# Kernel optimization log

Measured on AMD Instinct MI355X. Metric: run time of the kernel, lower is better.

## Reference

```python
import jax, jax.numpy as jnp
import numpy as np
import math

DIM = 1024
N_HEADS = 16
N_KV_HEADS = 8
HEAD_DIM = 64
HIDDEN = 4096
WINDOW = 512
NORM_EPS = 1e-5
QK_EPS = 1e-6


def get_alibi_slopes(n_heads):
    def _power_of_2(n):
        start = 2 ** (-2 ** (-(math.log2(n) - 3)))
        return [start * start ** i for i in range(n)]
    if math.log2(n_heads).is_integer():
        return _power_of_2(n_heads)
    closest = 2 ** math.floor(math.log2(n_heads))
    slopes = _power_of_2(closest)
    extra = _power_of_2(2 * closest)
    slopes.extend(extra[0::2][:n_heads - closest])
    return slopes


def layer_norm(x, w, eps):
    m = x.mean(-1, keepdims=True)
    v = ((x - m) ** 2).mean(-1, keepdims=True)
    return (x - m) * jax.lax.rsqrt(v + eps) * w


def setup_inputs() -> dict:
    key = jax.random.key(0)
    ks = jax.random.split(key, 16)
    s = 0.02
    return {
        "x": jax.random.normal(ks[0], (2, 2048, DIM), dtype=jnp.float32),
        "wq": jax.random.normal(ks[1], (N_HEADS * HEAD_DIM, DIM), dtype=jnp.float32) * s,
        "wk": jax.random.normal(ks[2], (N_KV_HEADS * HEAD_DIM, DIM), dtype=jnp.float32) * s,
        "wv": jax.random.normal(ks[3], (N_KV_HEADS * HEAD_DIM, DIM), dtype=jnp.float32) * s,
        "wo": jax.random.normal(ks[4], (DIM, N_HEADS * HEAD_DIM), dtype=jnp.float32) * s,
        "q_norm_w": jnp.ones((N_HEADS * HEAD_DIM,), dtype=jnp.float32),
        "k_norm_w": jnp.ones((N_KV_HEADS * HEAD_DIM,), dtype=jnp.float32),
        "attn_norm_w": jnp.ones((DIM,), dtype=jnp.float32),
        "ffn_norm_w": jnp.ones((DIM,), dtype=jnp.float32),
        "w1": jax.random.normal(ks[5], (HIDDEN, DIM), dtype=jnp.float32) * s,
        "w2": jax.random.normal(ks[6], (DIM, HIDDEN), dtype=jnp.float32) * s,
        "w3": jax.random.normal(ks[7], (HIDDEN, DIM), dtype=jnp.float32) * s,
        "attn_scale": jnp.full((DIM,), 1e-5, dtype=jnp.float32),
        "ffn_scale": jnp.full((DIM,), 1e-5, dtype=jnp.float32),
    }


def reference(x, wq, wk, wv, wo, q_norm_w, k_norm_w, attn_norm_w, ffn_norm_w,
              w1, w2, w3, attn_scale, ffn_scale):
    bsz, seqlen, _ = x.shape
    n_rep = N_HEADS // N_KV_HEADS

    h = layer_norm(x, attn_norm_w, NORM_EPS)
    q = layer_norm(h @ wq.T, q_norm_w, QK_EPS).reshape(bsz, seqlen, N_HEADS, HEAD_DIM).transpose(0, 2, 1, 3)
    k = layer_norm(h @ wk.T, k_norm_w, QK_EPS).reshape(bsz, seqlen, N_KV_HEADS, HEAD_DIM).transpose(0, 2, 1, 3)
    v = (h @ wv.T).reshape(bsz, seqlen, N_KV_HEADS, HEAD_DIM).transpose(0, 2, 1, 3)
    k = jnp.repeat(k, n_rep, axis=1)  # [b, H, s, hd]
    v = jnp.repeat(v, n_rep, axis=1)

    pos = jnp.arange(seqlen)
    dist = pos[None, :] - pos[:, None]  # dist[i, j] = j - i (as in the torch code)
    base = jnp.where((dist >= 0) & (dist <= WINDOW), 0.0, -jnp.inf)  # [s, s]
    slopes = jnp.asarray(get_alibi_slopes(N_HEADS), dtype=jnp.float32)
    alibi = -jnp.abs(slopes[:, None, None] * dist.astype(jnp.float32))  # [H, s, s]
    full_mask = base[None, :, :] + alibi  # [H, s, s]

    scores = jnp.einsum('bhqd,bhkd->bhqk', q, k) / math.sqrt(HEAD_DIM) + full_mask[None]
    attn = jax.nn.softmax(scores, axis=-1)
    out = jnp.einsum('bhqk,bhkd->bhqd', attn, v)
    out = out.transpose(0, 2, 1, 3).reshape(bsz, seqlen, N_HEADS * HEAD_DIM)
    x = x + (out @ wo.T) * attn_scale

    h2 = layer_norm(x, ffn_norm_w, NORM_EPS)
    ffn = (jax.nn.silu(h2 @ w1.T) * (h2 @ w3.T)) @ w2.T
    return x + ffn * ffn_scale
```

## Files before the change

kernel.cpp:

```cpp
#include <hip/hip_runtime.h>


typedef __bf16 bf16;
typedef __attribute__((ext_vector_type(8))) __bf16 bf16x8;
typedef __attribute__((ext_vector_type(4))) float f32x4;
typedef __attribute__((ext_vector_type(4))) short s16x4;

#define MFMA16(a, b, c) __builtin_amdgcn_mfma_f32_16x16x32_bf16(a, b, c, 0, 0, 0)

__device__ __forceinline__ void gload_lds16(const bf16* g, bf16* l) {
    __builtin_amdgcn_global_load_lds(
        (const __attribute__((address_space(1))) unsigned int*)g,
        (__attribute__((address_space(3))) unsigned int*)l, 16, 0, 0);
}

__global__ void sniff_kernel(const unsigned short* __restrict__ x, int* __restrict__ flag) {
    __shared__ int s;
    if (threadIdx.x == 0) s = 0;
    __syncthreads();
    int bad = 0;
#pragma unroll
    for (int i = 0; i < 16; ++i) {
        const unsigned short u = x[threadIdx.x * 16 + i];
        const int e = (u >> 7) & 0xFF;
        if (e >= 135) bad = 1;
    }
    if (bad) atomicOr(&s, 1);
    __syncthreads();
    if (threadIdx.x == 0) flag[0] = s;
}

__global__ void convert_all_kernel(const void* __restrict__ wq, const void* __restrict__ wk,
                                   const void* __restrict__ wv, const void* __restrict__ wo,
                                   const void* __restrict__ w1, const void* __restrict__ w3,
                                   const void* __restrict__ w2, bf16* __restrict__ dst,
                                   const int* __restrict__ flag) {
    const long e = ((long)blockIdx.x * 256 + threadIdx.x) * 4;
    const void* src; long off;
    if      (e < 1048576)  { src = wq; off = 0; }
    else if (e < 1572864)  { src = wk; off = 1048576; }
    else if (e < 2097152)  { src = wv; off = 1572864; }
    else if (e < 3145728)  { src = wo; off = 2097152; }
    else if (e < 7340032)  { src = w1; off = 3145728; }
    else if (e < 11534336) { src = w3; off = 7340032; }
    else                   { src = w2; off = 11534336; }
    if (flag[0] != 0) {
        const f32x4 v = *(const f32x4*)((const float*)src + (e - off));
        bf16 tmp[4];
#pragma unroll
        for (int j = 0; j < 4; ++j) tmp[j] = (bf16)v[j];
        *(s16x4*)(dst + e) = *(s16x4*)tmp;
    } else {
        *(s16x4*)(dst + e) = *(const s16x4*)((const short*)src + (e - off));
    }
}

__device__ __forceinline__ void ln_row(const void* in, const void* w, bf16* out,
                                       int row, int W, float eps, bool f32,
                                       int in_flv, int w_flv) {
    const int t = threadIdx.x;
    const int nch = W >> 3;
    const bool act = t < nch;
    float v[8];
    float s = 0.f, s2 = 0.f;
    if (act) {
        if (in_flv && f32) {
            const float* rp = (const float*)in + (size_t)row * W + t * 8;
            const f32x4 a = *(const f32x4*)rp, b = *(const f32x4*)(rp + 4);
#pragma unroll
            for (int j = 0; j < 4; ++j) { v[j] = a[j]; v[4 + j] = b[j]; }
        } else {
            const bf16x8 xv = *(const bf16x8*)((const bf16*)in + (size_t)row * W + t * 8);
#pragma unroll
            for (int j = 0; j < 8; ++j) v[j] = (float)xv[j];
        }
#pragma unroll
        for (int j = 0; j < 8; ++j) { s += v[j]; s2 += v[j] * v[j]; }
    }
#pragma unroll
    for (int off = 32; off; off >>= 1) { s += __shfl_xor(s, off); s2 += __shfl_xor(s2, off); }
    __shared__ float red[4];
    if ((t & 63) == 0) { red[(t >> 6) * 2] = s; red[(t >> 6) * 2 + 1] = s2; }
    __syncthreads();
    const float fs = red[0] + red[2], fs2 = red[1] + red[3];
    const float inw = 1.f / (float)W;
    const float mean = fs * inw;
    const float var = fs2 * inw - mean * mean;
    const float rstd = rsqrtf(var + eps);
    if (act) {
        float wv8[8];
        if (w_flv && f32) {
            const float* wp = (const float*)w + t * 8;
            const f32x4 a = *(const f32x4*)wp, b = *(const f32x4*)(wp + 4);
#pragma unroll
            for (int j = 0; j < 4; ++j) { wv8[j] = a[j]; wv8[4 + j] = b[j]; }
        } else {
            const bf16x8 ww = *(const bf16x8*)((const bf16*)w + t * 8);
#pragma unroll
            for (int j = 0; j < 8; ++j) wv8[j] = (float)ww[j];
        }
        bf16x8 ov;
#pragma unroll
        for (int j = 0; j < 8; ++j) ov[j] = (bf16)((v[j] - mean) * rstd * wv8[j]);
        *(bf16x8*)(out + (size_t)row * W + t * 8) = ov;
    }
}

__global__ void ln_kernel(const void* __restrict__ in, const void* __restrict__ w,
                          bf16* __restrict__ out, int W, float eps,
                          const int* __restrict__ flag, int in_flv, int w_flv) {
    ln_row(in, w, out, blockIdx.x, W, eps, flag[0] != 0, in_flv, w_flv);
}

__global__ void ln_qk_kernel(bf16* __restrict__ q, const void* __restrict__ qw,
                             bf16* __restrict__ kbuf, const void* __restrict__ kw,
                             const int* __restrict__ flag) {
    const bool f32 = flag[0] != 0;
    if (blockIdx.x < 4096)
        ln_row(q, qw, q, blockIdx.x, 1024, 1e-6f, f32, 0, 1);
    else
        ln_row(kbuf, kw, kbuf, blockIdx.x - 4096, 512, 1e-6f, f32, 0, 1);
}

__global__ void reduce_k(const bf16* __restrict__ p, const bf16* __restrict__ x1,
                         const void* __restrict__ scale, void* __restrict__ out,
                         const int* __restrict__ flag) {
    const bool f32 = flag[0] != 0;
    const size_t i8 = ((size_t)blockIdx.x * 256 + threadIdx.x) * 8;
    const int col = (int)(i8 & 1023);
    const bf16x8 a = *(const bf16x8*)(p + i8);
    const bf16x8 b = *(const bf16x8*)(p + 4194304 + i8);
    const bf16x8 r = *(const bf16x8*)(x1 + i8);
    float sc8[8];
    if (f32) {
        const f32x4 s0 = *(const f32x4*)((const float*)scale + col);
        const f32x4 s1 = *(const f32x4*)((const float*)scale + col + 4);
#pragma unroll
        for (int j = 0; j < 4; ++j) { sc8[j] = s0[j]; sc8[4 + j] = s1[j]; }
    } else {
        const bf16x8 sb = *(const bf16x8*)((const bf16*)scale + col);
#pragma unroll
        for (int j = 0; j < 8; ++j) sc8[j] = (float)sb[j];
    }
    float o[8];
#pragma unroll
    for (int j = 0; j < 8; ++j)
        o[j] = (float)r[j] + ((float)a[j] + (float)b[j]) * sc8[j];
    if (f32) {
        f32x4 o0, o1;
#pragma unroll
        for (int j = 0; j < 4; ++j) { o0[j] = o[j]; o1[j] = o[4 + j]; }
        *(f32x4*)((float*)out + i8) = o0;
        *(f32x4*)((float*)out + i8 + 4) = o1;
    } else {
        bf16x8 ov;
#pragma unroll
        for (int j = 0; j < 8; ++j) ov[j] = (bf16)o[j];
        *(bf16x8*)((bf16*)out + i8) = ov;
    }
}

template <int EPI, int NBUF, int SWZ, int SPLITK>
__global__ __launch_bounds__(512, 4)
void gemm2(const bf16* __restrict__ A, const bf16* __restrict__ B,
           void* __restrict__ Cout, const void* __restrict__ res,
           const void* __restrict__ scale, int M, int N, int K,
           const int* __restrict__ flag, int res_flv, int out_flv) {
    __shared__ bf16 LDS[NBUF * 8192];
    const bool f32 = flag[0] != 0;
    const int t = threadIdx.x;
    const int wv = t >> 6, ln = t & 63;
    const int qr = ln & 15, g = ln >> 4;
    const int wr = wv >> 2, wc = wv & 3;
    int bx = blockIdx.x, by = blockIdx.y;
    if (SWZ) {
        const int bid = by * gridDim.x + bx;
        const int g8 = bid & 7, m = bid >> 3;
        bx = m % gridDim.x;
        by = g8 + 8 * (m / gridDim.x);
    }
    const int row0 = by * 128, col0 = bx * 128;

    const int Koff = SPLITK ? (int)blockIdx.z * (K >> 1) : 0;
    const int Keff = SPLITK ? (K >> 1) : K;
    if (SPLITK) Cout = (void*)((bf16*)Cout + (size_t)blockIdx.z * ((size_t)M * N));

    f32x4 acc[4][2] = {};

    const int cx = ((t & 3) ^ ((t >> 2) & 3)) * 8;
    const bf16* aSrc = A + (size_t)(row0 + (t >> 2)) * K + Koff + cx;
    const bf16* bSrc = B + (size_t)(col0 + (t >> 2)) * K + Koff + cx;
    const int gx8 = (g ^ (qr & 3)) * 8;
    const int NIT = Keff >> 5;

#define STAGE(bi, k0)                                              \
    do {                                                           \
        bf16* lb = LDS + (bi) * 8192 + wv * 512;                   \
        gload_lds16(aSrc + (k0), lb);                              \
        gload_lds16(bSrc + (k0), lb + 4096);                       \
    } while (0)

#pragma unroll
    for (int pb = 0; pb < NBUF - 1; ++pb) STAGE(pb, pb * 32);
    if constexpr (NBUF == 3) asm volatile("s_waitcnt vmcnt(2)" ::: "memory");
    else                     asm volatile("s_waitcnt vmcnt(6)" ::: "memory");
    __builtin_amdgcn_s_barrier();
    __builtin_amdgcn_sched_barrier(0);

    int cur = 0, sb = NBUF - 1;
    for (int it = 0; it < NIT; ++it) {
        const bool more = (it + NBUF - 1) < NIT;
        if (more) STAGE(sb, (it + NBUF - 1) * 32);
        const bf16* bufA = LDS + cur * 8192;
        const bf16* bufB = bufA + 4096;
        bf16x8 af[4], bfr[2];
#pragma unroll
        for (int i = 0; i < 4; ++i)
            af[i] = *(const bf16x8*)&bufA[(wr * 64 + i * 16 + qr) * 32 + gx8];
#pragma unroll
        for (int j = 0; j < 2; ++j)
            bfr[j] = *(const bf16x8*)&bufB[(wc * 32 + j * 16 + qr) * 32 + gx8];
#pragma unroll
        for (int i = 0; i < 4; ++i)
#pragma unroll
            for (int j = 0; j < 2; ++j)
                acc[i][j] = MFMA16(af[i], bfr[j], acc[i][j]);
        if (more) {
            if constexpr (NBUF == 3) asm volatile("s_waitcnt vmcnt(2)" ::: "memory");
            else                     asm volatile("s_waitcnt vmcnt(6)" ::: "memory");
        } else {
            asm volatile("s_waitcnt vmcnt(0)" ::: "memory");
        }
        __builtin_amdgcn_s_barrier();
        __builtin_amdgcn_sched_barrier(0);
        cur = cur + 1 == NBUF ? 0 : cur + 1;
        sb  = sb + 1 == NBUF ? 0 : sb + 1;
    }
#undef STAGE

#pragma unroll
    for (int i = 0; i < 4; ++i) {
#pragma unroll
        for (int j = 0; j < 2; ++j) {
            const int rr0 = row0 + wr * 64 + i * 16 + g * 4;
            const int cc  = col0 + wc * 32 + j * 16 + qr;
            if (EPI == 4) {
                if (cc < 1024) {
#pragma unroll
                    for (int r = 0; r < 4; ++r)
                        ((bf16*)Cout)[(size_t)(rr0 + r) * 1024 + cc] = (bf16)acc[i][j][r];
                } else if (cc < 1536) {
#pragma unroll
                    for (int r = 0; r < 4; ++r)
                        ((bf16*)res)[(size_t)(rr0 + r) * 512 + (cc - 1024)] = (bf16)acc[i][j][r];
                } else {
                    const int kv = cc - 1536, kvh = kv >> 6, d = kv & 63;
                    const int bb = rr0 >> 11, s0 = rr0 & 2047;
                    bf16 tmp[4];
#pragma unroll
                    for (int r = 0; r < 4; ++r) tmp[r] = (bf16)acc[i][j][r];
                    *(s16x4*)((bf16*)scale + (((size_t)bb * 8 + kvh) * 64 + d) * 2048 + s0) = *(s16x4*)tmp;
                }
            } else {
                float scv = 0.f;
                if (EPI == 1)
                    scv = f32 ? ((const float*)scale)[cc] : (float)((const bf16*)scale)[cc];
#pragma unroll
                for (int r = 0; r < 4; ++r) {
                    const size_t idx = (size_t)(rr0 + r) * N + cc;
                    float vv = acc[i][j][r];
                    if (EPI == 1) {
                        const float rv = (res_flv && f32) ? ((const float*)res)[idx]
                                                          : (float)((const bf16*)res)[idx];
                        vv = rv + vv * scv;
                    }
                    if (EPI == 3) {
                        const float uv = (float)((const bf16*)res)[idx];
                        vv = uv / (1.f + __expf(-uv)) * vv;
                    }
                    if (out_flv && f32) ((float*)Cout)[idx] = vv;
                    else                ((bf16*)Cout)[idx] = (bf16)vv;
                }
            }
        }
    }
}

__global__ __launch_bounds__(512, 4)
void gemm_w13(const bf16* __restrict__ A, const bf16* __restrict__ B1,
              const bf16* __restrict__ B3, bf16* __restrict__ C,
              int M, int N, int K) {
    __shared__ bf16 LDS[3 * 12288];
    const int t = threadIdx.x;
    const int wv = t >> 6, ln = t & 63;
    const int qr = ln & 15, g = ln >> 4;
    const int wr = wv >> 2, wc = wv & 3;
    int bx, by;
    {
        const int bid = blockIdx.y * gridDim.x + blockIdx.x;
        const int xcd = bid & 7, m = bid >> 3;
        bx = xcd * 4 + (m & 3);
        by = m >> 2;
    }
    const int row0 = by * 128, col0 = bx * 128;

    f32x4 acc1[4][2] = {}, acc3[4][2] = {};

    const int cx = ((t & 3) ^ ((t >> 2) & 3)) * 8;
    const bf16* aSrc  = A  + (size_t)(row0 + (t >> 2)) * K + cx;
    const bf16* b1Src = B1 + (size_t)(col0 + (t >> 2)) * K + cx;
    const bf16* b3Src = B3 + (size_t)(col0 + (t >> 2)) * K + cx;
    const int gx8 = (g ^ (qr & 3)) * 8;
    const int NIT = K >> 5;

#define STAGEW(bi, k0)                                             \
    do {                                                           \
        bf16* lb = LDS + (bi) * 12288 + wv * 512;                  \
        gload_lds16(aSrc + (k0), lb);                              \
        gload_lds16(b1Src + (k0), lb + 4096);                      \
        gload_lds16(b3Src + (k0), lb + 8192);                      \
    } while (0)

    STAGEW(0, 0);
    STAGEW(1, 32);
    asm volatile("s_waitcnt vmcnt(3)" ::: "memory");
    __builtin_amdgcn_s_barrier();
    __builtin_amdgcn_sched_barrier(0);

    int cur = 0, sb = 2;
    for (int it = 0; it < NIT; ++it) {
        const bool more = (it + 2) < NIT;
        if (more) STAGEW(sb, (it + 2) * 32);
        const bf16* bufA  = LDS + cur * 12288;
        const bf16* bufB1 = bufA + 4096;
        const bf16* bufB3 = bufA + 8192;
        bf16x8 af[4], b1f[2], b3f[2];
#pragma unroll
        for (int i = 0; i < 4; ++i)
            af[i] = *(const bf16x8*)&bufA[(wr * 64 + i * 16 + qr) * 32 + gx8];
#pragma unroll
        for (int j = 0; j < 2; ++j) {
            b1f[j] = *(const bf16x8*)&bufB1[(wc * 32 + j * 16 + qr) * 32 + gx8];
            b3f[j] = *(const bf16x8*)&bufB3[(wc * 32 + j * 16 + qr) * 32 + gx8];
        }
#pragma unroll
        for (int i = 0; i < 4; ++i)
#pragma unroll
            for (int j = 0; j < 2; ++j) {
                acc1[i][j] = MFMA16(b1f[j], af[i], acc1[i][j]);
                acc3[i][j] = MFMA16(b3f[j], af[i], acc3[i][j]);
            }
        if (more) asm volatile("s_waitcnt vmcnt(3)" ::: "memory");
        else      asm volatile("s_waitcnt vmcnt(0)" ::: "memory");
        __builtin_amdgcn_s_barrier();
        __builtin_amdgcn_sched_barrier(0);
        cur = cur == 2 ? 0 : cur + 1;
        sb  = sb  == 2 ? 0 : sb  + 1;
    }
#undef STAGEW

#pragma unroll
    for (int i = 0; i < 4; ++i) {
        const int row = row0 + wr * 64 + i * 16 + qr;
#pragma unroll
        for (int j = 0; j < 2; ++j) {
            const int col = col0 + wc * 32 + j * 16 + g * 4;
            const size_t idx = (size_t)row * N + col;
            bf16 tmp[4];
#pragma unroll
            for (int r = 0; r < 4; ++r) {
                const float u1 = acc1[i][j][r];
                const float u3 = acc3[i][j][r];
                tmp[r] = (bf16)(u1 / (1.f + __expf(-u1)) * u3);
            }
            *(s16x4*)(C + idx) = *(s16x4*)tmp;
        }
    }
}

__global__ __launch_bounds__(512)
void attn_kernel(const bf16* __restrict__ qn, const bf16* __restrict__ kn,
                 const bf16* __restrict__ vt, bf16* __restrict__ aout) {
    __shared__ bf16 SH[3 * 4096];
    const int t = threadIdx.x, wv = t >> 6, ln = t & 63;
    const int qr = ln & 15, g = ln >> 4;
    const int kvh = blockIdx.y, b = blockIdx.z;
    const int hh = wv & 1, h = kvh * 2 + hh;
    const int qsub = wv >> 1;
    const int q0blk = blockIdx.x * 64;
    const int qa = q0blk + qsub * 16 + qr;
    const float slope = exp2f(-0.5f * (float)(h + 1));

    const bf16* qrow = qn + ((size_t)(b * 2048 + qa)) * 1024 + h * 64;
    const bf16x8 qb0 = *(const bf16x8*)(qrow + g * 8);
    const bf16x8 qb1 = *(const bf16x8*)(qrow + 32 + g * 8);

    const bf16* kbase = kn + (size_t)b * 2048 * 512 + kvh * 64;
    const bf16* vbase = vt + ((size_t)(b * 8 + kvh) * 64) * 2048;

    const bool isK = t < 256;
    const int ts = t & 255;
    const int krow_l = ts >> 3;
    const int kcsrc  = (ts & 7) ^ ((ts >> 3) & 7);
    const int vd     = ts >> 2;
    const int vcsrc  = (ts & 3) ^ ((ts >> 2) & 3);
    const bf16* kgsrc = kbase + kcsrc * 8;
    const bf16* vgsrc = vbase + (size_t)vd * 2048;
    bf16* ldst = isK ? (SH + wv * 512) : (SH + 2048 + (wv - 4) * 512);

#define STAGE_T(kts, bi)                                           \
    do {                                                           \
        if (isK) {                                                 \
            int ksrc = (kts) + krow_l;                             \
            ksrc = ksrc > 2047 ? 2047 : ksrc;                      \
            gload_lds16(kgsrc + (size_t)ksrc * 512, ldst + (bi) * 4096); \
        } else {                                                   \
            int vsrc = (kts) + vcsrc * 8;                          \
            vsrc = vsrc > 2040 ? 2040 : vsrc;                      \
            gload_lds16(vgsrc + vsrc, ldst + (bi) * 4096);         \
        }                                                          \
    } while (0)

    STAGE_T(q0blk, 0);
    STAGE_T(q0blk + 32, 1);
    asm volatile("s_waitcnt vmcnt(1)" ::: "memory");
    __builtin_amdgcn_s_barrier();
    __builtin_amdgcn_sched_barrier(0);

    f32x4 o[4] = {};
    float mrun = -1e29f, lsum = 0.f;
    int cur = 0, sb = 2;

    for (int it = 0; it < 18; ++it) {
        const int kt = q0blk + it * 32;
        const bool more = (it + 2) < 18;
        if (more) STAGE_T(kt + 64, sb);
        const bf16* Kb = SH + cur * 4096;
        const bf16* Vb = Kb + 2048;

        f32x4 sc[2] = {f32x4{0, 0, 0, 0}, f32x4{0, 0, 0, 0}};
#pragma unroll
        for (int ks = 0; ks < 2; ++ks) {
            const int lrow = ks * 16 + qr;
            const int sw = (lrow & 7) * 8;
            sc[ks] = MFMA16(*(const bf16x8*)&Kb[lrow * 64 + (((g) * 8) ^ sw)],        qb0, sc[ks]);
            sc[ks] = MFMA16(*(const bf16x8*)&Kb[lrow * 64 + (((4 + g) * 8) ^ sw)],    qb1, sc[ks]);
        }
        float s[2][4], p[2][4];
        float tmax = -1e30f;
#pragma unroll
        for (int ks = 0; ks < 2; ++ks)
#pragma unroll
            for (int r = 0; r < 4; ++r) {
                const int key = kt + ks * 16 + g * 4 + r;
                const int dist = key - qa;
                const bool valid = (dist >= 0) && (dist <= 512) && (key < 2048);
                const float sv = valid ? sc[ks][r] * 0.125f - slope * (float)dist : -1e30f;
                s[ks][r] = sv;
                tmax = fmaxf(tmax, sv);
            }
        tmax = fmaxf(tmax, __shfl_xor(tmax, 16));
        tmax = fmaxf(tmax, __shfl_xor(tmax, 32));
        const float mnew = fmaxf(mrun, tmax);
        const float alpha = __expf(mrun - mnew);
        mrun = mnew;
        float ps = 0.f;
#pragma unroll
        for (int ks = 0; ks < 2; ++ks)
#pragma unroll
            for (int r = 0; r < 4; ++r) { p[ks][r] = __expf(s[ks][r] - mnew); ps += p[ks][r]; }
        lsum = lsum * alpha + ps;
#pragma unroll
        for (int fd = 0; fd < 4; ++fd) o[fd] *= alpha;

        bf16x8 pb;
#pragma unroll
        for (int j = 0; j < 8; ++j) {
            const int srcl = (((2 * g + (j >> 2)) & 3) << 4) | qr;
            const float v0 = __shfl(p[0][j & 3], srcl);
            const float v1 = __shfl(p[1][j & 3], srcl);
            pb[j] = (bf16)((g & 2) ? v1 : v0);
        }
#pragma unroll
        for (int fd = 0; fd < 4; ++fd) {
            const int d = fd * 16 + qr;
            const bf16x8 va = *(const bf16x8*)&Vb[d * 32 + ((g ^ (d & 3)) * 8)];
            o[fd] = MFMA16(va, pb, o[fd]);
        }

        if (more) asm volatile("s_waitcnt vmcnt(1)" ::: "memory");
        else      asm volatile("s_waitcnt vmcnt(0)" ::: "memory");
        __builtin_amdgcn_s_barrier();
        __builtin_amdgcn_sched_barrier(0);
        cur = cur == 2 ? 0 : cur + 1;
        sb  = sb  == 2 ? 0 : sb  + 1;
    }
#undef STAGE_T

    float lt = lsum + __shfl_xor(lsum, 16);
    lt += __shfl_xor(lt, 32);
    lt = fmaxf(lt, 1e-30f);
    const float inv = 1.f / lt;
    bf16* orow = aout + ((size_t)(b * 2048 + qa)) * 1024 + h * 64;
#pragma unroll
    for (int fd = 0; fd < 4; ++fd) {
        bf16 tmp[4];
#pragma unroll
        for (int r = 0; r < 4; ++r) tmp[r] = (bf16)(o[fd][r] * inv);
        *(s16x4*)(orow + fd * 16 + g * 4) = *(s16x4*)tmp;
    }
}

extern "C" void kernel_launch(void* const* d_in, const int* in_sizes, int n_in,
                              void* d_out, int out_size, void* d_ws, size_t ws_size,
                              hipStream_t stream) {
    int* flag = (int*)d_ws;
    bf16* base = (bf16*)d_ws + 64;
    bf16* h    = base;
    bf16* q    = h + 4194304;
    bf16* kbuf = q + 4194304;
    bf16* vtb  = kbuf + 2097152;
    bf16* aout = vtb + 2097152;
    bf16* u    = aout + 4194304;
    bf16* wcv  = u + 16777216;

    bf16* woc = wcv + 2097152;
    bf16* w1c = wcv + 3145728;
    bf16* w3c = wcv + 7340032;
    bf16* w2c = wcv + 11534336;

    const dim3 blk(512);
    sniff_kernel<<<1, 256, 0, stream>>>((const unsigned short*)d_in[0], flag);
    convert_all_kernel<<<15360, 256, 0, stream>>>(
        d_in[1], d_in[2], d_in[3], d_in[4], d_in[9], d_in[11], d_in[10], wcv, flag);

    ln_kernel<<<4096, 128, 0, stream>>>(d_in[0], d_in[7], h, 1024, 1e-5f, flag, 1, 1);
    gemm2<4, 3, 0, 0><<<dim3(16, 32), blk, 0, stream>>>(h, wcv, q, kbuf, vtb, 4096, 2048, 1024, flag, 0, 0);
    ln_qk_kernel<<<8192, 128, 0, stream>>>(q, d_in[5], kbuf, d_in[6], flag);
    attn_kernel<<<dim3(32, 8, 2), dim3(512), 0, stream>>>(q, kbuf, vtb, aout);
    gemm2<1, 3, 1, 0><<<dim3(8, 32), blk, 0, stream>>>(aout, woc, q, d_in[0], d_in[12], 4096, 1024, 1024, flag, 1, 0);
    ln_kernel<<<4096, 128, 0, stream>>>(q, d_in[8], h, 1024, 1e-5f, flag, 0, 1);
    gemm_w13<<<dim3(32, 32), blk, 0, stream>>>(h, w1c, w3c, u, 4096, 4096, 1024);
    gemm2<0, 5, 1, 1><<<dim3(8, 32, 2), blk, 0, stream>>>(u, w2c, kbuf, nullptr, nullptr, 4096, 1024, 4096, flag, 0, 0);
    reduce_k<<<2048, 256, 0, stream>>>(kbuf, q, d_in[13], d_out, flag);
}
```

Measured before the change: 246.9 us.

## Enlarge w1/w3 GEMM tile to 256 rows with 4-stage split-phase pipeline

The fused w1/w3 SwiGLU GEMM now computes a 256x128 tile per block instead of 128x128, with each wave covering 64x64. This raises arithmetic intensity per staged byte and halves the grid. The LDS ring grows to four slots, and loads are split: A-loads are issued before the w1 MFMAs and B-loads before the w3 MFMAs, with setprio raised around the MFMA bursts. Costs are more accumulator registers (occupancy hint drops to 2), more LDS, and fewer blocks per CU.

```diff
diff --git a/kernel.cpp b/kernel.cpp
--- a/kernel.cpp
+++ b/kernel.cpp
@@ -286,15 +286,15 @@
     }
 }
 
-__global__ __launch_bounds__(512, 4)
+__global__ __launch_bounds__(512, 2)
 void gemm_w13(const bf16* __restrict__ A, const bf16* __restrict__ B1,
               const bf16* __restrict__ B3, bf16* __restrict__ C,
               int M, int N, int K) {
-    __shared__ bf16 LDS[3 * 12288];
+    __shared__ bf16 LDS[4 * 16384];
     const int t = threadIdx.x;
     const int wv = t >> 6, ln = t & 63;
     const int qr = ln & 15, g = ln >> 4;
-    const int wr = wv >> 2, wc = wv & 3;
+    const int wr = wv >> 1, wc = wv & 1;
     int bx, by;
     {
         const int bid = blockIdx.y * gridDim.x + blockIdx.x;
@@ -302,69 +302,81 @@
         bx = xcd * 4 + (m & 3);
         by = m >> 2;
     }
-    const int row0 = by * 128, col0 = bx * 128;
-
-    f32x4 acc1[4][2] = {}, acc3[4][2] = {};
+    const int row0 = by * 256, col0 = bx * 128;
+
+    f32x4 acc1[4][4] = {}, acc3[4][4] = {};
 
     const int cx = ((t & 3) ^ ((t >> 2) & 3)) * 8;
-    const bf16* aSrc  = A  + (size_t)(row0 + (t >> 2)) * K + cx;
+    const bf16* aSrc0 = A  + (size_t)(row0 + (t >> 2)) * K + cx;
+    const bf16* aSrc1 = A  + (size_t)(row0 + 128 + (t >> 2)) * K + cx;
     const bf16* b1Src = B1 + (size_t)(col0 + (t >> 2)) * K + cx;
     const bf16* b3Src = B3 + (size_t)(col0 + (t >> 2)) * K + cx;
     const int gx8 = (g ^ (qr & 3)) * 8;
-    const int NIT = K >> 5;
-
-#define STAGEW(bi, k0)                                             \
-    do {                                                           \
-        bf16* lb = LDS + (bi) * 12288 + wv * 512;                  \
-        gload_lds16(aSrc + (k0), lb);                              \
-        gload_lds16(b1Src + (k0), lb + 4096);                      \
-        gload_lds16(b3Src + (k0), lb + 8192);                      \
-    } while (0)
-
-    STAGEW(0, 0);
-    STAGEW(1, 32);
-    asm volatile("s_waitcnt vmcnt(3)" ::: "memory");
+    const int NU = K >> 5;
+
+#define ST_A0(s, k0) gload_lds16(aSrc0 + (k0), LDS + (s) * 16384 + wv * 512)
+#define ST_A1(s, k0) gload_lds16(aSrc1 + (k0), LDS + (s) * 16384 + 4096 + wv * 512)
+#define ST_B1(s, k0) gload_lds16(b1Src + (k0), LDS + (s) * 16384 + 8192 + wv * 512)
+#define ST_B3(s, k0) gload_lds16(b3Src + (k0), LDS + (s) * 16384 + 12288 + wv * 512)
+
+    ST_A0(0, 0);  ST_A1(0, 0);  ST_B1(0, 0);  ST_B3(0, 0);
+    ST_A0(1, 32); ST_A1(1, 32); ST_B1(1, 32); ST_B3(1, 32);
+    asm volatile("s_waitcnt vmcnt(4)" ::: "memory");
     __builtin_amdgcn_s_barrier();
     __builtin_amdgcn_sched_barrier(0);
 
-    int cur = 0, sb = 2;
-    for (int it = 0; it < NIT; ++it) {
-        const bool more = (it + 2) < NIT;
-        if (more) STAGEW(sb, (it + 2) * 32);
-        const bf16* bufA  = LDS + cur * 12288;
-        const bf16* bufB1 = bufA + 4096;
-        const bf16* bufB3 = bufA + 8192;
-        bf16x8 af[4], b1f[2], b3f[2];
+    for (int u = 0; u < NU; ++u) {
+        const int su = u & 3;
+        const bf16* slot = LDS + su * 16384;
+        const bool more = (u + 2) < NU;
+        const int kn = (u + 2) * 32;
+        const int sn = (u + 2) & 3;
+
+        if (more) { ST_A0(sn, kn); ST_A1(sn, kn); }
+        bf16x8 af[4], bf1[4];
 #pragma unroll
         for (int i = 0; i < 4; ++i)
-            af[i] = *(const bf16x8*)&bufA[(wr * 64 + i * 16 + qr) * 32 + gx8];
-#pragma unroll
-        for (int j = 0; j < 2; ++j) {
-            b1f[j] = *(const bf16x8*)&bufB1[(wc * 32 + j * 16 + qr) * 32 + gx8];
-            b3f[j] = *(const bf16x8*)&bufB3[(wc * 32 + j * 16 + qr) * 32 + gx8];
-        }
+            af[i] = *(const bf16x8*)&slot[(wr * 64 + i * 16 + qr) * 32 + gx8];
+#pragma unroll
+        for (int j = 0; j < 4; ++j)
+            bf1[j] = *(const bf16x8*)&slot[8192 + (wc * 64 + j * 16 + qr) * 32 + gx8];
+        __builtin_amdgcn_s_setprio(1);
 #pragma unroll
         for (int i = 0; i < 4; ++i)
 #pragma unroll
-            for (int j = 0; j < 2; ++j) {
-                acc1[i][j] = MFMA16(b1f[j], af[i], acc1[i][j]);
-                acc3[i][j] = MFMA16(b3f[j], af[i], acc3[i][j]);
-            }
-        if (more) asm volatile("s_waitcnt vmcnt(3)" ::: "memory");
+            for (int j = 0; j < 4; ++j)
+                acc1[i][j] = MFMA16(bf1[j], af[i], acc1[i][j]);
+        __builtin_amdgcn_s_setprio(0);
+
+        if (more) { ST_B1(sn, kn); ST_B3(sn, kn); }
+        bf16x8 bf3[4];
+#pragma unroll
+        for (int j = 0; j < 4; ++j)
+            bf3[j] = *(const bf16x8*)&slot[12288 + (wc * 64 + j * 16 + qr) * 32 + gx8];
+        __builtin_amdgcn_s_setprio(1);
+#pragma unroll
+        for (int i = 0; i < 4; ++i)
+#pragma unroll
+            for (int j = 0; j < 4; ++j)
+                acc3[i][j] = MFMA16(bf3[j], af[i], acc3[i][j]);
+        __builtin_amdgcn_s_setprio(0);
+
+        if (more) asm volatile("s_waitcnt vmcnt(4)" ::: "memory");
         else      asm volatile("s_waitcnt vmcnt(0)" ::: "memory");
         __builtin_amdgcn_s_barrier();
         __builtin_amdgcn_sched_barrier(0);
-        cur = cur == 2 ? 0 : cur + 1;
-        sb  = sb  == 2 ? 0 : sb  + 1;
-    }
-#undef STAGEW
+    }
+#undef ST_A0
+#undef ST_A1
+#undef ST_B1
+#undef ST_B3
 
 #pragma unroll
     for (int i = 0; i < 4; ++i) {
         const int row = row0 + wr * 64 + i * 16 + qr;
 #pragma unroll
-        for (int j = 0; j < 2; ++j) {
-            const int col = col0 + wc * 32 + j * 16 + g * 4;
+        for (int j = 0; j < 4; ++j) {
+            const int col = col0 + wc * 64 + j * 16 + g * 4;
             const size_t idx = (size_t)row * N + col;
             bf16 tmp[4];
 #pragma unroll
@@ -540,7 +552,7 @@
     attn_kernel<<<dim3(32, 8, 2), dim3(512), 0, stream>>>(q, kbuf, vtb, aout);
     gemm2<1, 3, 1, 0><<<dim3(8, 32), blk, 0, stream>>>(aout, woc, q, d_in[0], d_in[12], 4096, 1024, 1024, flag, 1, 0);
     ln_kernel<<<4096, 128, 0, stream>>>(q, d_in[8], h, 1024, 1e-5f, flag, 0, 1);
-    gemm_w13<<<dim3(32, 32), blk, 0, stream>>>(h, w1c, w3c, u, 4096, 4096, 1024);
+    gemm_w13<<<dim3(32, 16), blk, 0, stream>>>(h, w1c, w3c, u, 4096, 4096, 1024);
     gemm2<0, 5, 1, 1><<<dim3(8, 32, 2), blk, 0, stream>>>(u, w2c, kbuf, nullptr, nullptr, 4096, 1024, 4096, flag, 0, 0);
     reduce_k<<<2048, 256, 0, stream>>>(kbuf, q, d_in[13], d_out, flag);
 }
```

After: 243.8 us. No clear change (-1.2%).
